# Kernel tuning notes

Hardware: AMD Instinct MI355X
Metric: run time of the kernel (lower is better)

The kernel has to match this reference:

```python
import jax, jax.numpy as jnp
import numpy as np

B, T, I, H, O = 2048, 512, 1, 64, 1


def setup_inputs() -> dict:
    key = jax.random.key(0)
    ks = jax.random.split(key, 7)
    k = 1.0 / np.sqrt(H)  # PyTorch default uniform init bound
    u = lambda kk, sh: jax.random.uniform(kk, sh, jnp.float32, -k, k)
    return {
        "x": jax.random.normal(ks[0], (B, T, I), jnp.float32),
        "w_ih": u(ks[1], (4 * H, I)),   # gate order: i, f, g, o (PyTorch)
        "w_hh": u(ks[2], (4 * H, H)),
        "b_ih": u(ks[3], (4 * H,)),
        "b_hh": u(ks[4], (4 * H,)),
        "w_lin": u(ks[5], (O, H)),
        "b_lin": u(ks[6], (O,)),
    }


def _lstm_last_h(x, w_ih, w_hh, b_ih, b_hh):
    """Single-layer LSTM (PyTorch gate order i,f,g,o), returns h at the last step."""
    Bsz = x.shape[0]
    Hs = w_hh.shape[1]
    # Precompute input contribution for all timesteps: [B, T, 4H]
    gx_all = jnp.einsum('bti,gi->btg', x, w_ih) + b_ih + b_hh

    def step(carry, gx):
        h, c = carry
        g = gx + h @ w_hh.T  # [B, 4H]
        i, f, gg, o = jnp.split(g, 4, axis=-1)
        i = jax.nn.sigmoid(i)
        f = jax.nn.sigmoid(f)
        gg = jnp.tanh(gg)
        o = jax.nn.sigmoid(o)
        c = f * c + i * gg
        h = o * jnp.tanh(c)
        return (h, c), None

    h0 = jnp.zeros((Bsz, Hs), x.dtype)
    (h_last, _), _ = jax.lax.scan(step, (h0, h0), jnp.swapaxes(gx_all, 0, 1))
    return h_last  # == out[:, -1, :]


def reference(x, w_ih, w_hh, b_ih, b_hh, w_lin, b_lin):
    h = _lstm_last_h(x, w_ih, w_hh, b_ih, b_hh)
    return h @ w_lin.T + b_lin  # [B, O]
```

## Files before the change

kernel.cpp:

```cpp
#include <hip/hip_runtime.h>


typedef float    f32x4 __attribute__((ext_vector_type(4)));
typedef _Float16 f16x8 __attribute__((ext_vector_type(8)));
typedef _Float16 f16x4 __attribute__((ext_vector_type(4)));

namespace {
constexpr int Bsz = 2048;
constexpr int Tsz = 512;
constexpr int NBW = 16;
}

__device__ __forceinline__ float rcp_f(float v)  { return __builtin_amdgcn_rcpf(v); }
__device__ __forceinline__ float exp2_f(float v) { return __builtin_amdgcn_exp2f(v); }

__device__ __forceinline__ float sigm_s(float gs) {
    return rcp_f(1.0f + exp2_f(gs));
}
__device__ __forceinline__ float tanh_s(float gs) {
    return fmaf(2.0f, rcp_f(1.0f + exp2_f(gs)), -1.0f);
}
__device__ __forceinline__ float tanh_plain(float v) {
    return fmaf(2.0f, rcp_f(1.0f + exp2_f(v * -2.88539008178f)), -1.0f);
}

__global__ __launch_bounds__(256, 1)
void lstm_v5(const float* __restrict__ x,
             const float* __restrict__ w_ih,
             const float* __restrict__ w_hh,
             const float* __restrict__ b_ih,
             const float* __restrict__ b_hh,
             const float* __restrict__ w_lin,
             const float* __restrict__ b_lin,
             float* __restrict__ out)
{
    __shared__ __align__(16) char hAb[2][16 * 128];

    const int tid = threadIdx.x;
    const int wv  = tid >> 6;
    const int ln  = tid & 63;
    const int row = ln & 15;
    const int grp = ln >> 4;
    const int b0  = blockIdx.x * NBW;

    constexpr float LOG2E = 1.44269504089f;

    f16x8 Wf[4][2];
    float wihc[4][4], biasc[4][4];
    #pragma unroll
    for (int g = 0; g < 4; ++g) {
        const float s = (g == 2) ? (-2.0f * LOG2E) : (-LOG2E);
        const float* wrow = w_hh + (size_t)(g * 64 + 16 * wv + row) * 64;
        #pragma unroll
        for (int kc = 0; kc < 2; ++kc) {
            const float4 a = ((const float4*)wrow)[kc * 8 + grp * 2 + 0];
            const float4 b = ((const float4*)wrow)[kc * 8 + grp * 2 + 1];
            f16x8 w;
            w[0] = (_Float16)(a.x * s); w[1] = (_Float16)(a.y * s);
            w[2] = (_Float16)(a.z * s); w[3] = (_Float16)(a.w * s);
            w[4] = (_Float16)(b.x * s); w[5] = (_Float16)(b.y * s);
            w[6] = (_Float16)(b.z * s); w[7] = (_Float16)(b.w * s);
            Wf[g][kc] = w;
        }
        #pragma unroll
        for (int reg = 0; reg < 4; ++reg) {
            const int gt = g * 64 + 16 * wv + 4 * grp + reg;
            wihc[g][reg]  = w_ih[gt] * s;
            biasc[g][reg] = (b_ih[gt] + b_hh[gt]) * s;
        }
    }

    float wlinc[4];
    #pragma unroll
    for (int reg = 0; reg < 4; ++reg)
        wlinc[reg] = w_lin[16 * wv + 4 * grp + reg];

    const int sw    = (row & 7) << 4;
    const int boff0 = row * 128 + ((0 * 64 + grp * 16) ^ sw);
    const int boff1 = row * 128 + ((1 * 64 + grp * 16) ^ sw);
    const int hwoff = row * 128 + (((32 * wv + 8 * grp)) ^ sw);

    reinterpret_cast<float2*>(&hAb[0][0])[tid] = make_float2(0.0f, 0.0f);

    const float4* xp4 = (const float4*)(x + (size_t)(b0 + row) * Tsz);
    float4 xcur = xp4[0];

    float c[4] = {0.f, 0.f, 0.f, 0.f};
    float h[4] = {0.f, 0.f, 0.f, 0.f};

    __syncthreads();

    for (int t4 = 0; t4 < Tsz / 4; ++t4) {
        const float4 xnxt = xp4[(t4 < Tsz / 4 - 1) ? (t4 + 1) : (Tsz / 4 - 1)];

        #pragma unroll
        for (int s = 0; s < 4; ++s) {
            const int rp = s & 1;
            const int wp = rp ^ 1;
            const float xs = (s == 0) ? xcur.x : (s == 1) ? xcur.y
                           : (s == 2) ? xcur.z : xcur.w;

            const f16x8 B0 = *(const f16x8*)(hAb[rp] + boff0);
            const f16x8 B1 = *(const f16x8*)(hAb[rp] + boff1);

            f32x4 acc[4];
            #pragma unroll
            for (int g = 0; g < 4; ++g) {
                #pragma unroll
                for (int reg = 0; reg < 4; ++reg)
                    acc[g][reg] = fmaf(xs, wihc[g][reg], biasc[g][reg]);
            }
            #pragma unroll
            for (int g = 0; g < 4; ++g)
                acc[g] = __builtin_amdgcn_mfma_f32_16x16x32_f16(Wf[g][0], B0, acc[g], 0, 0, 0);
            #pragma unroll
            for (int g = 0; g < 4; ++g)
                acc[g] = __builtin_amdgcn_mfma_f32_16x16x32_f16(Wf[g][1], B1, acc[g], 0, 0, 0);

            f16x4 hp;
            #pragma unroll
            for (int reg = 0; reg < 4; ++reg) {
                const float ig = sigm_s(acc[0][reg]);
                const float fg = sigm_s(acc[1][reg]);
                const float tg = tanh_s(acc[2][reg]);
                const float og = sigm_s(acc[3][reg]);
                c[reg] = fmaf(fg, c[reg], ig * tg);
                h[reg] = og * tanh_plain(c[reg]);
                hp[reg] = (_Float16)h[reg];
            }
            *(f16x4*)(hAb[wp] + hwoff) = hp;

            __syncthreads();
        }
        xcur = xnxt;
    }

    float p = h[0] * wlinc[0] + h[1] * wlinc[1] + h[2] * wlinc[2] + h[3] * wlinc[3];
    p += __shfl_xor(p, 16, 64);
    p += __shfl_xor(p, 32, 64);
    float* part = reinterpret_cast<float*>(&hAb[0][0]);
    if (ln < 16) part[wv * 16 + ln] = p;
    __syncthreads();
    if (tid < 16)
        out[b0 + tid] = part[tid] + part[16 + tid] + part[32 + tid] +
                        part[48 + tid] + b_lin[0];
}

extern "C" void kernel_launch(void* const* d_in, const int* in_sizes, int n_in,
                              void* d_out, int out_size, void* d_ws, size_t ws_size,
                              hipStream_t stream) {
    const float* x     = (const float*)d_in[0];
    const float* w_ih  = (const float*)d_in[1];
    const float* w_hh  = (const float*)d_in[2];
    const float* b_ih  = (const float*)d_in[3];
    const float* b_hh  = (const float*)d_in[4];
    const float* w_lin = (const float*)d_in[5];
    const float* b_lin = (const float*)d_in[6];
    float* out = (float*)d_out;

    dim3 grid(Bsz / NBW);
    dim3 block(256);
    lstm_v5<<<grid, block, 0, stream>>>(x, w_ih, w_hh, b_ih, b_hh,
                                        w_lin, b_lin, out);
}
```

Before: 297.8 us.

## Shrink batch tile to four rows and redistribute gate math via LDS

Reduces the batch rows per block from 16 to 4, so the grid has four times as many blocks, and allows two blocks per CU. MFMA gate outputs for the valid rows are scattered to LDS so that each lane computes the LSTM cell update for a single (batch, hidden) element, which cuts per-lane transcendental work. This aims to fill all CUs and shorten the serial per-step critical path. In exchange, most MFMA columns do wasted work, and each step adds an extra LDS round trip.

```diff
diff --git a/kernel.cpp b/kernel.cpp
--- a/kernel.cpp
+++ b/kernel.cpp
@@ -3,12 +3,11 @@
 
 typedef float    f32x4 __attribute__((ext_vector_type(4)));
 typedef _Float16 f16x8 __attribute__((ext_vector_type(8)));
-typedef _Float16 f16x4 __attribute__((ext_vector_type(4)));
 
 namespace {
 constexpr int Bsz = 2048;
 constexpr int Tsz = 512;
-constexpr int NBW = 16;
+constexpr int NBW = 4;
 }
 
 __device__ __forceinline__ float rcp_f(float v)  { return __builtin_amdgcn_rcpf(v); }
@@ -24,8 +23,8 @@
     return fmaf(2.0f, rcp_f(1.0f + exp2_f(v * -2.88539008178f)), -1.0f);
 }
 
-__global__ __launch_bounds__(256, 1)
-void lstm_v5(const float* __restrict__ x,
+__global__ __launch_bounds__(256, 2)
+void lstm_v6(const float* __restrict__ x,
              const float* __restrict__ w_ih,
              const float* __restrict__ w_hh,
              const float* __restrict__ b_ih,
@@ -35,6 +34,8 @@
              float* __restrict__ out)
 {
     __shared__ __align__(16) char hAb[2][16 * 128];
+    __shared__ __align__(16) char cg[4][1024];
+    __shared__ float part[16];
 
     const int tid = threadIdx.x;
     const int wv  = tid >> 6;
@@ -70,23 +71,27 @@
         }
     }
 
-    float wlinc[4];
-    #pragma unroll
-    for (int reg = 0; reg < 4; ++reg)
-        wlinc[reg] = w_lin[16 * wv + 4 * grp + reg];
-
     const int sw    = (row & 7) << 4;
     const int boff0 = row * 128 + ((0 * 64 + grp * 16) ^ sw);
     const int boff1 = row * 128 + ((1 * 64 + grp * 16) ^ sw);
-    const int hwoff = row * 128 + (((32 * wv + 8 * grp)) ^ sw);
 
-    reinterpret_cast<float2*>(&hAb[0][0])[tid] = make_float2(0.0f, 0.0f);
+    int cwoff[4];
+    #pragma unroll
+    for (int reg = 0; reg < 4; ++reg)
+        cwoff[reg] = wv * 1024 + row * 256 + ((((grp << 2) + reg) * 16) ^ (row << 4));
+    const int pb  = ln & 3;
+    const int jl  = ln >> 2;
+    const int croff = wv * 1024 + pb * 256 + ((jl * 16) ^ (pb << 4));
+    const int j_own = 16 * wv + jl;
+    const int hwoff = pb * 128 + ((2 * j_own) ^ (pb << 4));
+    const float wlin = w_lin[j_own];
 
-    const float4* xp4 = (const float4*)(x + (size_t)(b0 + row) * Tsz);
+    ((float4*)hAb)[tid] = make_float4(0.f, 0.f, 0.f, 0.f);
+
+    const float4* xp4 = (const float4*)(x + (size_t)(b0 + (ln & 3)) * Tsz);
     float4 xcur = xp4[0];
 
-    float c[4] = {0.f, 0.f, 0.f, 0.f};
-    float h[4] = {0.f, 0.f, 0.f, 0.f};
+    float c = 0.0f, h = 0.0f;
 
     __syncthreads();
 
@@ -117,33 +122,41 @@
             for (int g = 0; g < 4; ++g)
                 acc[g] = __builtin_amdgcn_mfma_f32_16x16x32_f16(Wf[g][1], B1, acc[g], 0, 0, 0);
 
-            f16x4 hp;
-            #pragma unroll
-            for (int reg = 0; reg < 4; ++reg) {
-                const float ig = sigm_s(acc[0][reg]);
-                const float fg = sigm_s(acc[1][reg]);
-                const float tg = tanh_s(acc[2][reg]);
-                const float og = sigm_s(acc[3][reg]);
-                c[reg] = fmaf(fg, c[reg], ig * tg);
-                h[reg] = og * tanh_plain(c[reg]);
-                hp[reg] = (_Float16)h[reg];
+            if (row < 4) {
+                #pragma unroll
+                for (int reg = 0; reg < 4; ++reg) {
+                    f32x4 cw;
+                    cw[0] = acc[0][reg]; cw[1] = acc[1][reg];
+                    cw[2] = acc[2][reg]; cw[3] = acc[3][reg];
+                    *(f32x4*)(cg[0] + cwoff[reg]) = cw;
+                }
             }
-            *(f16x4*)(hAb[wp] + hwoff) = hp;
+            asm volatile("s_waitcnt lgkmcnt(0)" ::: "memory");
+            const f32x4 g4 = *(const f32x4*)(cg[0] + croff);
+
+            const float ig = sigm_s(g4[0]);
+            const float fg = sigm_s(g4[1]);
+            const float tg = tanh_s(g4[2]);
+            const float og = sigm_s(g4[3]);
+            c = fmaf(fg, c, ig * tg);
+            h = og * tanh_plain(c);
+
+            *(_Float16*)(hAb[wp] + hwoff) = (_Float16)h;
 
             __syncthreads();
         }
         xcur = xnxt;
     }
 
-    float p = h[0] * wlinc[0] + h[1] * wlinc[1] + h[2] * wlinc[2] + h[3] * wlinc[3];
-    p += __shfl_xor(p, 16, 64);
-    p += __shfl_xor(p, 32, 64);
-    float* part = reinterpret_cast<float*>(&hAb[0][0]);
-    if (ln < 16) part[wv * 16 + ln] = p;
+    float p = h * wlin;
+    #pragma unroll
+    for (int off = 4; off < 64; off <<= 1)
+        p += __shfl_xor(p, off, 64);
+    if (ln < 4) part[wv * 4 + ln] = p;
     __syncthreads();
-    if (tid < 16)
-        out[b0 + tid] = part[tid] + part[16 + tid] + part[32 + tid] +
-                        part[48 + tid] + b_lin[0];
+    if (tid < 4)
+        out[b0 + tid] = part[tid] + part[4 + tid] +
+                        part[8 + tid] + part[12 + tid] + b_lin[0];
 }
 
 extern "C" void kernel_launch(void* const* d_in, const int* in_sizes, int n_in,
@@ -160,6 +173,6 @@
 
     dim3 grid(Bsz / NBW);
     dim3 block(256);
-    lstm_v5<<<grid, block, 0, stream>>>(x, w_ih, w_hh, b_ih, b_hh,
+    lstm_v6<<<grid, block, 0, stream>>>(x, w_ih, w_hh, b_ih, b_hh,
                                         w_lin, b_lin, out);
 }
```

New measurement: 318.1 us. +6.8%, slower.
